# Optimization experiments

Hardware: AMD Instinct MI355X
Metric: run time of the kernel (lower is better)

## Reference

```python
import jax, jax.numpy as jnp
import numpy as np

B, D, H, W = 32, 64, 32, 32
M = 1024  # codebook_size


def setup_inputs() -> dict:
    key = jax.random.key(0)
    k1, k2, k3 = jax.random.split(key, 3)
    z = jax.random.normal(k1, (B, D, H, W), dtype=jnp.float32)
    codebook = jax.random.normal(k2, (M, D), dtype=jnp.float32)
    noise = jax.random.normal(k3, (B * H * W, D), dtype=jnp.float32)
    return {"z": z, "codebook": codebook, "noise": noise}


def reference(z, codebook, noise):
    b, d, h, w = z.shape
    n = b * h * w
    # (B,D,H,W) -> (B,H,W,D) -> (N,D)
    zf = jnp.transpose(z, (0, 2, 3, 1)).reshape(n, d)
    x2 = jnp.sum(zf * zf, axis=1, keepdims=True)          # (N,1)
    y2 = jnp.sum(codebook * codebook, axis=1)[None, :]    # (1,M)
    dist = x2 + y2 - 2.0 * (zf @ codebook.T)              # (N,M)
    dist_min = jnp.min(dist, axis=1, keepdims=True)       # (N,1)
    ind = jnp.argmin(dist, axis=1)                        # (N,) int
    # noise substitution: unit-norm random direction scaled by sqrt(min dist)
    nrm = jnp.maximum(jnp.linalg.norm(noise, axis=-1, keepdims=True), 1e-9)
    q_error = noise / nrm * jnp.sqrt(jnp.maximum(dist_min, 0.0))
    z_q = zf + q_error                                    # (N,D)
    # torch: z_q.view(B, D, H*W) is a raw memory reshape of the (B*H*W, D) buffer
    z_q_view = z_q.reshape(b, d, h * w)                   # (B,D,HW)
    # loss = mean over (B,HW,HW) of z_q_view^T @ z_q_view
    #      = sum_b sum_d (sum_n z_q_view[b,d,n])^2 / (B * HW^2)  (no HWxHW intermediate)
    s = jnp.sum(z_q_view, axis=2)                         # (B,D)
    hw = h * w
    loss = jnp.sum(s * s) / (b * hw * hw)
    z_q_out = jnp.transpose(z_q.reshape(b, h, w, d), (0, 3, 1, 2))  # (B,D,H,W)
    return z_q_out, loss, ind
```

## Files before the change

### kernel.cpp

```cpp
#include <hip/hip_runtime.h>
#include <hip/hip_bf16.h>

#define BB 32
#define DD 64
#define HW 1024
#define NN 32768
#define MM 1024

typedef _Float16 half8 __attribute__((ext_vector_type(8)));
typedef float    floatx4 __attribute__((ext_vector_type(4)));

#define MFMA16(a, b, c) __builtin_amdgcn_mfma_f32_16x16x32_f16((a), (b), (c), 0, 0, 0)

#define LO_SCALE   2048.0f
#define LO_INV     (1.0f / 2048.0f)

__global__ void k_prep(const float* __restrict__ cb,
                       _Float16* __restrict__ ch,
                       _Float16* __restrict__ cl,
                       float* __restrict__ y2,
                       float* __restrict__ loss_slot) {
    int u = blockIdx.x * blockDim.x + threadIdx.x;
    if (u == 0) *loss_slot = 0.0f;

    if (u < 64 * 2 * 64) {
        int lane  = u & 63;
        int kstep = (u >> 6) & 1;
        int mtile = u >> 7;
        int m  = mtile * 16 + (lane & 15);
        int d0 = kstep * 32 + ((lane >> 4) & 3) * 8;
        const float* src = cb + (size_t)m * DD + d0;
        half8 h, l;
#pragma unroll
        for (int j = 0; j < 8; ++j) {
            float x = -2.0f * src[j];
            _Float16 hi = (_Float16)x;
            _Float16 lo = (_Float16)((x - (float)hi) * LO_SCALE);
            h[j] = hi;
            l[j] = lo;
        }
        *(half8*)(ch + (size_t)u * 8) = h;
        *(half8*)(cl + (size_t)u * 8) = l;
    }

    if (u < MM) {
        const float4* c4 = (const float4*)(cb + (size_t)u * DD);
        float s = 0.f;
#pragma unroll
        for (int k = 0; k < 16; ++k) {
            float4 v = c4[k];
            s += v.x * v.x + v.y * v.y + v.z * v.z + v.w * v.w;
        }
        y2[u] = s;
    }
}

__global__ __launch_bounds__(512, 4) void k_main(const float* __restrict__ z,
                                                 const float* __restrict__ noise,
                                                 const _Float16* __restrict__ ch,
                                                 const _Float16* __restrict__ cl,
                                                 const float* __restrict__ y2,
                                                 float* __restrict__ zq,
                                                 float* __restrict__ ind_out,
                                                 float* __restrict__ loss_slot) {
    __shared__ float zt[64][65];
    __shared__ float nt[64][65];
    __shared__ float y2s[MM];
    __shared__ float x2p[64][8];
    __shared__ float snorm[64];
    __shared__ float scale_s[64];
    __shared__ float bestv_s[4][64];
    __shared__ int   besti_s[4][64];
    __shared__ float partials[512];
    __shared__ float sq[4];

    const int t    = threadIdx.x;
    const int lane = t & 63;
    const int wv   = t >> 6;
    const int nth  = wv & 1;
    const int cq   = wv >> 1;
    const int quad = lane >> 4;
    const int col  = lane & 15;
    const int blk  = blockIdx.x;
    const int b    = blk >> 4;
    const int hw0  = (blk & 15) << 6;

    const float* zbase = z + ((size_t)b << 16) + hw0;

    for (int i = t; i < 64 * 64; i += 512) {
        int d = i >> 6, r = i & 63;
        zt[r][d] = zbase[(size_t)d * HW + r];
    }
    for (int i = t; i < MM; i += 512) y2s[i] = y2[i];

    {
        const float4* noise4 = (const float4*)noise;
        const size_t base4 = (size_t)blk * 1024;
#pragma unroll
        for (int k = 0; k < 2; ++k) {
            int v = t + 512 * k;
            float4 vv = noise4[base4 + v];
            int c  = v >> 4;
            int d0 = (v & 15) << 2;
            nt[d0 + 0][c] = vv.x;
            nt[d0 + 1][c] = vv.y;
            nt[d0 + 2][c] = vv.z;
            nt[d0 + 3][c] = vv.w;
            float p = vv.x * vv.x + vv.y * vv.y + vv.z * vv.z + vv.w * vv.w;
            p += __shfl_xor(p, 1);
            p += __shfl_xor(p, 2);
            p += __shfl_xor(p, 4);
            p += __shfl_xor(p, 8);
            if ((t & 15) == 0) snorm[c] = p;
        }
    }
    __syncthreads();

    {
        int row = t & 63, seg = t >> 6;
        float s = 0.f;
#pragma unroll
        for (int j = 0; j < 8; ++j) {
            float v = zt[row][seg * 8 + j];
            s = __builtin_fmaf(v, v, s);
        }
        x2p[row][seg] = s;
    }

    half8 ah[2][2], al[2][2];
#pragma unroll
    for (int nt2 = 0; nt2 < 2; ++nt2) {
        int row = nth * 32 + nt2 * 16 + col;
#pragma unroll
        for (int ks = 0; ks < 2; ++ks) {
            int d0 = ks * 32 + quad * 8;
            half8 h, l;
#pragma unroll
            for (int j = 0; j < 8; ++j) {
                float x = zt[row][d0 + j];
                _Float16 hi = (_Float16)x;
                _Float16 lo = (_Float16)((x - (float)hi) * LO_SCALE);
                h[j] = hi;
                l[j] = lo;
            }
            ah[nt2][ks] = h;
            al[nt2][ks] = l;
        }
    }
    __syncthreads();

    const half8* ch8 = (const half8*)ch;
    const half8* cl8 = (const half8*)cl;

    float best[8];
    int   bmt[8];
#pragma unroll
    for (int s = 0; s < 8; ++s) { best[s] = 1e30f; bmt[s] = 0; }

    const int mt0 = cq * 16;
    half8 bh0 = ch8[((mt0 * 2 + 0) << 6) + lane];
    half8 bl0 = cl8[((mt0 * 2 + 0) << 6) + lane];
    half8 bh1 = ch8[((mt0 * 2 + 1) << 6) + lane];
    half8 bl1 = cl8[((mt0 * 2 + 1) << 6) + lane];

#pragma unroll 2
    for (int i = 0; i < 16; ++i) {
        const int mt  = mt0 + i;
        const int mtn = mt + (i < 15 ? 1 : 0);
        half8 nh0 = ch8[((mtn * 2 + 0) << 6) + lane];
        half8 nl0 = cl8[((mtn * 2 + 0) << 6) + lane];
        half8 nh1 = ch8[((mtn * 2 + 1) << 6) + lane];
        half8 nl1 = cl8[((mtn * 2 + 1) << 6) + lane];

        float y2v = y2s[(mt << 4) + col];
        floatx4 a1[2], a2[2];
#pragma unroll
        for (int n2 = 0; n2 < 2; ++n2) {
            floatx4 i1 = {y2v, y2v, y2v, y2v};
            floatx4 i2 = {0.f, 0.f, 0.f, 0.f};
            a1[n2] = i1;
            a2[n2] = i2;
        }
#pragma unroll
        for (int n2 = 0; n2 < 2; ++n2) {
            a1[n2] = MFMA16(ah[n2][0], bh0, a1[n2]);
            a2[n2] = MFMA16(al[n2][0], bh0, a2[n2]);
            a2[n2] = MFMA16(ah[n2][0], bl0, a2[n2]);
            a1[n2] = MFMA16(ah[n2][1], bh1, a1[n2]);
            a2[n2] = MFMA16(al[n2][1], bh1, a2[n2]);
            a2[n2] = MFMA16(ah[n2][1], bl1, a2[n2]);
        }
#pragma unroll
        for (int n2 = 0; n2 < 2; ++n2) {
#pragma unroll
            for (int r = 0; r < 4; ++r) {
                float v = __builtin_fmaf(a2[n2][r], LO_INV, a1[n2][r]);
                int s = n2 * 4 + r;
                bool c = v < best[s];
                best[s] = c ? v : best[s];
                bmt[s]  = c ? mt : bmt[s];
            }
        }
        bh0 = nh0; bl0 = nl0; bh1 = nh1; bl1 = nl1;
    }

#pragma unroll
    for (int n2 = 0; n2 < 2; ++n2) {
#pragma unroll
        for (int r = 0; r < 4; ++r) {
            int s = n2 * 4 + r;
            float v  = best[s];
            int  idx = bmt[s] * 16 + col;
#pragma unroll
            for (int mask = 1; mask <= 8; mask <<= 1) {
                float v2 = __shfl_xor(v, mask);
                int   i2 = __shfl_xor(idx, mask);
                if (v2 < v || (v2 == v && i2 < idx)) { v = v2; idx = i2; }
            }
            if (col == 0) {
                int rl = nth * 32 + n2 * 16 + quad * 4 + r;
                bestv_s[cq][rl] = v;
                besti_s[cq][rl] = idx;
            }
        }
    }
    __syncthreads();

    if (t < 64) {
        float bv = bestv_s[0][t];
        int   bi = besti_s[0][t];
#pragma unroll
        for (int w = 1; w < 4; ++w) {
            float v = bestv_s[w][t];
            int   ix = besti_s[w][t];
            if (v < bv || (v == bv && ix < bi)) { bv = v; bi = ix; }
        }
        float x2 = 0.f;
#pragma unroll
        for (int s = 0; s < 8; ++s) x2 += x2p[t][s];
        float dm = x2 + bv;
        int n = (blk << 6) + t;
        ind_out[n] = (float)bi;
        float nr = fmaxf(sqrtf(snorm[t]), 1e-9f);
        scale_s[t] = sqrtf(fmaxf(dm, 0.f)) / nr;
    }
    __syncthreads();

    float acc = 0.f;
    const size_t obase = ((size_t)b << 16) + hw0;
#pragma unroll
    for (int it = 0; it < 8; ++it) {
        int flat = it * 512 + t;
        int d = flat >> 6;
        int c = t & 63;
        float v = zt[c][d] + nt[d][c] * scale_s[c];
        zq[obase + (size_t)d * HW + c] = v;
        acc += v;
    }

    partials[t] = acc;
    __syncthreads();
    if (t < 4) {
        float s = 0.f;
        for (int g = 0; g < 8; ++g)
            for (int j = 0; j < 16; ++j)
                s += partials[g * 64 + t * 16 + j];
        sq[t] = s * s;
    }
    __syncthreads();
    if (t == 0) {
        float contrib = (sq[0] + sq[1] + sq[2] + sq[3]) * (1.0f / 33554432.0f);
        atomicAdd(loss_slot, contrib);
    }
}

extern "C" void kernel_launch(void* const* d_in, const int* in_sizes, int n_in,
                              void* d_out, int out_size, void* d_ws, size_t ws_size,
                              hipStream_t stream) {
    const float* z        = (const float*)d_in[0];
    const float* codebook = (const float*)d_in[1];
    const float* noise    = (const float*)d_in[2];

    float* out      = (float*)d_out;
    float* zq_out   = out;
    float* loss_ptr = out + 2097152;
    float* ind_out  = out + 2097153;

    float* y2       = (float*)d_ws;
    _Float16* ch    = (_Float16*)(y2 + MM);
    _Float16* cl    = ch + 65536;

    k_prep<<<16,  512, 0, stream>>>(codebook, ch, cl, y2, loss_ptr);
    k_main<<<512, 512, 0, stream>>>(z, noise, ch, cl, y2,
                                    zq_out, ind_out, loss_ptr);
}
```

Baseline: 98.72 us.

## Give each wave all 64 rows and an 8-tile codebook slice with deeper prefetch

```diff
diff --git a/kernel.cpp b/kernel.cpp
--- a/kernel.cpp
+++ b/kernel.cpp
@@ -55,7 +55,7 @@
     }
 }
 
-__global__ __launch_bounds__(512, 4) void k_main(const float* __restrict__ z,
+__global__ __launch_bounds__(512, 2) void k_main(const float* __restrict__ z,
                                                  const float* __restrict__ noise,
                                                  const _Float16* __restrict__ ch,
                                                  const _Float16* __restrict__ cl,
@@ -69,16 +69,14 @@
     __shared__ float x2p[64][8];
     __shared__ float snorm[64];
     __shared__ float scale_s[64];
-    __shared__ float bestv_s[4][64];
-    __shared__ int   besti_s[4][64];
+    __shared__ float bestv_s[8][64];
+    __shared__ int   besti_s[8][64];
     __shared__ float partials[512];
     __shared__ float sq[4];
 
     const int t    = threadIdx.x;
     const int lane = t & 63;
     const int wv   = t >> 6;
-    const int nth  = wv & 1;
-    const int cq   = wv >> 1;
     const int quad = lane >> 4;
     const int col  = lane & 15;
     const int blk  = blockIdx.x;
@@ -127,10 +125,10 @@
         x2p[row][seg] = s;
     }
 
-    half8 ah[2][2], al[2][2];
-#pragma unroll
-    for (int nt2 = 0; nt2 < 2; ++nt2) {
-        int row = nth * 32 + nt2 * 16 + col;
+    half8 ah[4][2], al[4][2];
+#pragma unroll
+    for (int ntl = 0; ntl < 4; ++ntl) {
+        int row = ntl * 16 + col;
 #pragma unroll
         for (int ks = 0; ks < 2; ++ks) {
             int d0 = ks * 32 + quad * 8;
@@ -143,8 +141,8 @@
                 h[j] = hi;
                 l[j] = lo;
             }
-            ah[nt2][ks] = h;
-            al[nt2][ks] = l;
+            ah[ntl][ks] = h;
+            al[ntl][ks] = l;
         }
     }
     __syncthreads();
@@ -152,63 +150,70 @@
     const half8* ch8 = (const half8*)ch;
     const half8* cl8 = (const half8*)cl;
 
-    float best[8];
-    int   bmt[8];
-#pragma unroll
-    for (int s = 0; s < 8; ++s) { best[s] = 1e30f; bmt[s] = 0; }
-
-    const int mt0 = cq * 16;
-    half8 bh0 = ch8[((mt0 * 2 + 0) << 6) + lane];
-    half8 bl0 = cl8[((mt0 * 2 + 0) << 6) + lane];
-    half8 bh1 = ch8[((mt0 * 2 + 1) << 6) + lane];
-    half8 bl1 = cl8[((mt0 * 2 + 1) << 6) + lane];
-
-#pragma unroll 2
-    for (int i = 0; i < 16; ++i) {
-        const int mt  = mt0 + i;
-        const int mtn = mt + (i < 15 ? 1 : 0);
-        half8 nh0 = ch8[((mtn * 2 + 0) << 6) + lane];
-        half8 nl0 = cl8[((mtn * 2 + 0) << 6) + lane];
-        half8 nh1 = ch8[((mtn * 2 + 1) << 6) + lane];
-        half8 nl1 = cl8[((mtn * 2 + 1) << 6) + lane];
-
+    float best[16];
+    int   bmt[16];
+#pragma unroll
+    for (int s = 0; s < 16; ++s) { best[s] = 1e30f; bmt[s] = 0; }
+
+    const int mt0 = wv * 8;
+
+    half8 h0[8], l0[8], h1[8], l1[8];
+#pragma unroll
+    for (int i = 0; i < 2; ++i) {
+        int mt = mt0 + i;
+        h0[i] = ch8[((mt * 2 + 0) << 6) + lane];
+        l0[i] = cl8[((mt * 2 + 0) << 6) + lane];
+        h1[i] = ch8[((mt * 2 + 1) << 6) + lane];
+        l1[i] = cl8[((mt * 2 + 1) << 6) + lane];
+    }
+
+#pragma unroll
+    for (int i = 0; i < 8; ++i) {
+        if (i + 2 < 8) {
+            int mtp = mt0 + i + 2;
+            h0[i + 2] = ch8[((mtp * 2 + 0) << 6) + lane];
+            l0[i + 2] = cl8[((mtp * 2 + 0) << 6) + lane];
+            h1[i + 2] = ch8[((mtp * 2 + 1) << 6) + lane];
+            l1[i + 2] = cl8[((mtp * 2 + 1) << 6) + lane];
+        }
+
+        const int mt = mt0 + i;
         float y2v = y2s[(mt << 4) + col];
-        floatx4 a1[2], a2[2];
-#pragma unroll
-        for (int n2 = 0; n2 < 2; ++n2) {
+        floatx4 a1[4], a2[4];
+#pragma unroll
+        for (int ntl = 0; ntl < 4; ++ntl) {
             floatx4 i1 = {y2v, y2v, y2v, y2v};
             floatx4 i2 = {0.f, 0.f, 0.f, 0.f};
-            a1[n2] = i1;
-            a2[n2] = i2;
-        }
-#pragma unroll
-        for (int n2 = 0; n2 < 2; ++n2) {
-            a1[n2] = MFMA16(ah[n2][0], bh0, a1[n2]);
-            a2[n2] = MFMA16(al[n2][0], bh0, a2[n2]);
-            a2[n2] = MFMA16(ah[n2][0], bl0, a2[n2]);
-            a1[n2] = MFMA16(ah[n2][1], bh1, a1[n2]);
-            a2[n2] = MFMA16(al[n2][1], bh1, a2[n2]);
-            a2[n2] = MFMA16(ah[n2][1], bl1, a2[n2]);
-        }
-#pragma unroll
-        for (int n2 = 0; n2 < 2; ++n2) {
+            a1[ntl] = i1;
+            a2[ntl] = i2;
+        }
+#pragma unroll
+        for (int ntl = 0; ntl < 4; ++ntl) {
+            a1[ntl] = MFMA16(ah[ntl][0], h0[i], a1[ntl]);
+            a2[ntl] = MFMA16(al[ntl][0], h0[i], a2[ntl]);
+            a2[ntl] = MFMA16(ah[ntl][0], l0[i], a2[ntl]);
+            a1[ntl] = MFMA16(ah[ntl][1], h1[i], a1[ntl]);
+            a2[ntl] = MFMA16(al[ntl][1], h1[i], a2[ntl]);
+            a2[ntl] = MFMA16(ah[ntl][1], l1[i], a2[ntl]);
+        }
+#pragma unroll
+        for (int ntl = 0; ntl < 4; ++ntl) {
 #pragma unroll
             for (int r = 0; r < 4; ++r) {
-                float v = __builtin_fmaf(a2[n2][r], LO_INV, a1[n2][r]);
-                int s = n2 * 4 + r;
+                float v = __builtin_fmaf(a2[ntl][r], LO_INV, a1[ntl][r]);
+                int s = ntl * 4 + r;
                 bool c = v < best[s];
                 best[s] = c ? v : best[s];
                 bmt[s]  = c ? mt : bmt[s];
             }
         }
-        bh0 = nh0; bl0 = nl0; bh1 = nh1; bl1 = nl1;
-    }
-
-#pragma unroll
-    for (int n2 = 0; n2 < 2; ++n2) {
+    }
+
+#pragma unroll
+    for (int ntl = 0; ntl < 4; ++ntl) {
 #pragma unroll
         for (int r = 0; r < 4; ++r) {
-            int s = n2 * 4 + r;
+            int s = ntl * 4 + r;
             float v  = best[s];
             int  idx = bmt[s] * 16 + col;
 #pragma unroll
@@ -218,9 +223,9 @@
                 if (v2 < v || (v2 == v && i2 < idx)) { v = v2; idx = i2; }
             }
             if (col == 0) {
-                int rl = nth * 32 + n2 * 16 + quad * 4 + r;
-                bestv_s[cq][rl] = v;
-                besti_s[cq][rl] = idx;
+                int rl = ntl * 16 + quad * 4 + r;
+                bestv_s[wv][rl] = v;
+                besti_s[wv][rl] = idx;
             }
         }
     }
@@ -230,7 +235,7 @@
         float bv = bestv_s[0][t];
         int   bi = besti_s[0][t];
 #pragma unroll
-        for (int w = 1; w < 4; ++w) {
+        for (int w = 1; w < 8; ++w) {
             float v = bestv_s[w][t];
             int   ix = besti_s[w][t];
             if (v < bv || (v == bv && ix < bi)) { bv = v; bi = ix; }
```

Result: slower. 153.5 us (+55.5%).

## Stage codebook tiles through double-buffered shared memory shared by row-halves

Applied to the files above, without the earlier changes.

```diff
diff --git a/kernel.cpp b/kernel.cpp
--- a/kernel.cpp
+++ b/kernel.cpp
@@ -73,17 +73,33 @@
     __shared__ int   besti_s[4][64];
     __shared__ float partials[512];
     __shared__ float sq[4];
+    __shared__ _Float16 bufB[2 * 8192];
 
     const int t    = threadIdx.x;
     const int lane = t & 63;
     const int wv   = t >> 6;
-    const int nth  = wv & 1;
-    const int cq   = wv >> 1;
+    const int mi   = wv & 3;
+    const int rh   = wv >> 2;
     const int quad = lane >> 4;
     const int col  = lane & 15;
     const int blk  = blockIdx.x;
     const int b    = blk >> 4;
     const int hw0  = (blk & 15) << 6;
+
+    const half8* ch8 = (const half8*)ch;
+    const half8* cl8 = (const half8*)cl;
+    half8* bh8 = (half8*)bufB;
+
+    const int e0 = t, e1 = 512 + t;
+    const int r0 = e0 >> 6, j0 = e0 & 63;
+    const int r1 = e1 >> 6, j1 = e1 & 63;
+    const half8* s0base = ((r0 & 1) ? cl8 : ch8) + ((r0 >> 1) << 6) + j0;
+    const half8* s1base = ((r1 & 1) ? cl8 : ch8) + ((r1 >> 1) << 6) + j1;
+
+    half8 st0[2], st1[2];
+
+    st0[0] = s0base[0];
+    st1[0] = s1base[0];
 
     const float* zbase = z + ((size_t)b << 16) + hw0;
 
@@ -129,8 +145,8 @@
 
     half8 ah[2][2], al[2][2];
 #pragma unroll
-    for (int nt2 = 0; nt2 < 2; ++nt2) {
-        int row = nth * 32 + nt2 * 16 + col;
+    for (int n2 = 0; n2 < 2; ++n2) {
+        int row = rh * 32 + n2 * 16 + col;
 #pragma unroll
         for (int ks = 0; ks < 2; ++ks) {
             int d0 = ks * 32 + quad * 8;
@@ -143,35 +159,32 @@
                 h[j] = hi;
                 l[j] = lo;
             }
-            ah[nt2][ks] = h;
-            al[nt2][ks] = l;
-        }
-    }
-    __syncthreads();
-
-    const half8* ch8 = (const half8*)ch;
-    const half8* cl8 = (const half8*)cl;
+            ah[n2][ks] = h;
+            al[n2][ks] = l;
+        }
+    }
+
+    bh8[e0] = st0[0];
+    bh8[e1] = st1[0];
+    st0[1] = s0base[512];
+    st1[1] = s1base[512];
+    __syncthreads();
 
     float best[8];
     int   bmt[8];
 #pragma unroll
     for (int s = 0; s < 8; ++s) { best[s] = 1e30f; bmt[s] = 0; }
 
-    const int mt0 = cq * 16;
-    half8 bh0 = ch8[((mt0 * 2 + 0) << 6) + lane];
-    half8 bl0 = cl8[((mt0 * 2 + 0) << 6) + lane];
-    half8 bh1 = ch8[((mt0 * 2 + 1) << 6) + lane];
-    half8 bl1 = cl8[((mt0 * 2 + 1) << 6) + lane];
-
-#pragma unroll 2
-    for (int i = 0; i < 16; ++i) {
-        const int mt  = mt0 + i;
-        const int mtn = mt + (i < 15 ? 1 : 0);
-        half8 nh0 = ch8[((mtn * 2 + 0) << 6) + lane];
-        half8 nl0 = cl8[((mtn * 2 + 0) << 6) + lane];
-        half8 nh1 = ch8[((mtn * 2 + 1) << 6) + lane];
-        half8 nl1 = cl8[((mtn * 2 + 1) << 6) + lane];
-
+#pragma unroll
+    for (int c = 0; c < 16; ++c) {
+        const int bi = c & 1;
+        const half8* bb = bh8 + (bi << 10);
+        half8 h0 = bb[(((mi << 2) + 0) << 6) + lane];
+        half8 l0 = bb[(((mi << 2) + 1) << 6) + lane];
+        half8 h1 = bb[(((mi << 2) + 2) << 6) + lane];
+        half8 l1 = bb[(((mi << 2) + 3) << 6) + lane];
+
+        const int mt = c * 4 + mi;
         float y2v = y2s[(mt << 4) + col];
         floatx4 a1[2], a2[2];
 #pragma unroll
@@ -183,12 +196,12 @@
         }
 #pragma unroll
         for (int n2 = 0; n2 < 2; ++n2) {
-            a1[n2] = MFMA16(ah[n2][0], bh0, a1[n2]);
-            a2[n2] = MFMA16(al[n2][0], bh0, a2[n2]);
-            a2[n2] = MFMA16(ah[n2][0], bl0, a2[n2]);
-            a1[n2] = MFMA16(ah[n2][1], bh1, a1[n2]);
-            a2[n2] = MFMA16(al[n2][1], bh1, a2[n2]);
-            a2[n2] = MFMA16(ah[n2][1], bl1, a2[n2]);
+            a1[n2] = MFMA16(ah[n2][0], h0, a1[n2]);
+            a2[n2] = MFMA16(al[n2][0], h0, a2[n2]);
+            a2[n2] = MFMA16(ah[n2][0], l0, a2[n2]);
+            a1[n2] = MFMA16(ah[n2][1], h1, a1[n2]);
+            a2[n2] = MFMA16(al[n2][1], h1, a2[n2]);
+            a2[n2] = MFMA16(ah[n2][1], l1, a2[n2]);
         }
 #pragma unroll
         for (int n2 = 0; n2 < 2; ++n2) {
@@ -196,12 +209,23 @@
             for (int r = 0; r < 4; ++r) {
                 float v = __builtin_fmaf(a2[n2][r], LO_INV, a1[n2][r]);
                 int s = n2 * 4 + r;
-                bool c = v < best[s];
-                best[s] = c ? v : best[s];
-                bmt[s]  = c ? mt : bmt[s];
-            }
-        }
-        bh0 = nh0; bl0 = nl0; bh1 = nh1; bl1 = nl1;
+                bool cc = v < best[s];
+                best[s] = cc ? v : best[s];
+                bmt[s]  = cc ? mt : bmt[s];
+            }
+        }
+
+        if (c < 15) {
+            const int pnext = (c + 1) & 1;
+            bh8[(pnext << 10) + e0] = st0[pnext];
+            bh8[(pnext << 10) + e1] = st1[pnext];
+            if (c < 14) {
+                const int pn2 = (c + 2) & 1;
+                st0[pn2] = s0base[(c + 2) << 9];
+                st1[pn2] = s1base[(c + 2) << 9];
+            }
+        }
+        __syncthreads();
     }
 
 #pragma unroll
@@ -218,9 +242,9 @@
                 if (v2 < v || (v2 == v && i2 < idx)) { v = v2; idx = i2; }
             }
             if (col == 0) {
-                int rl = nth * 32 + n2 * 16 + quad * 4 + r;
-                bestv_s[cq][rl] = v;
-                besti_s[cq][rl] = idx;
+                int rl = rh * 32 + n2 * 16 + quad * 4 + r;
+                bestv_s[mi][rl] = v;
+                besti_s[mi][rl] = idx;
             }
         }
     }
```

Result: slower. 232.4 us (+135.4%).
